# Optimization experiments

Hardware: AMD Instinct MI355X
Metric: run time of the kernel (lower is better)

## Reference

```python
import jax, jax.numpy as jnp
import numpy as np

B, D, L, E, R = 16384, 2048, 3, 8, 64


def setup_inputs() -> dict:
    key = jax.random.key(0)
    k1, k2, k3, k4 = jax.random.split(key, 4)
    scale = 1.0 / np.sqrt(D)  # ~ PyTorch Linear default init scale
    X0 = jax.random.normal(k1, (B, D), dtype=jnp.float32)
    U = jax.random.normal(k2, (L, E, R, D), dtype=jnp.float32) * scale
    V = jax.random.normal(k3, (L, E, R, D), dtype=jnp.float32) * scale
    Wg = jax.random.normal(k4, (L, E, D), dtype=jnp.float32) * scale
    bg = jnp.zeros((L, E), dtype=jnp.float32)
    return {"X0": X0, "U": U, "V": V, "Wg": Wg, "bg": bg}


def reference(X0, U, V, Wg, bg):
    # X0: (B, D); U, V: (L, E, R, D); Wg: (L, E, D); bg: (L, E)
    Xi = X0
    num_layers = U.shape[0]
    for l in range(num_layers):  # small fixed layer count
        gate = jax.nn.softmax(jnp.einsum('bd,ed->be', Xi, Wg[l]) + bg[l], axis=1)  # (B, E)
        Uo = jnp.einsum('bd,erd->ber', Xi, U[l])  # (B, E, R)
        Vo = jnp.einsum('bd,erd->ber', Xi, V[l])  # (B, E, R)
        expert_out = jnp.sum(Uo * Vo, axis=2)     # (B, E) low-rank bilinear forms
        xw = jnp.sum(expert_out * gate, axis=1, keepdims=True)  # (B, 1)
        Xi = Xi + X0 * xw  # residual cross update (dropout=0, eval mode)
    return Xi
```

## Files before the change

### kernel.cpp

```cpp
#include <hip/hip_runtime.h>
#include <hip/hip_bf16.h>

#define BDIM 16384
#define DDIM 2048
#define LNUM 3
#define ENUM 8
#define NP 24

#define BM 256
#define BK 64
#define NT (DDIM / BK)

typedef _Float16 f16x8 __attribute__((ext_vector_type(8)));
typedef _Float16 f16x4 __attribute__((ext_vector_type(4)));
typedef float f32x4 __attribute__((ext_vector_type(4)));

__global__ void cvt_w_kernel(const float* __restrict__ U, const float* __restrict__ V,
                             const float* __restrict__ Wg,
                             _Float16* __restrict__ Wh, _Float16* __restrict__ Wgh) {
    if (blockIdx.x >= 6144) {
        int f = (int)((blockIdx.x - 6144) * blockDim.x + threadIdx.x);
        float4 v = ((const float4*)Wg)[f];
        f16x4 h = { (_Float16)v.x, (_Float16)v.y, (_Float16)v.z, (_Float16)v.w };
        ((f16x4*)Wgh)[f] = h;
        return;
    }
    size_t f = (size_t)blockIdx.x * blockDim.x + threadIdx.x;
    size_t elem = f * 4;
    int d   = (int)(elem & (DDIM - 1));
    int row = (int)((elem >> 11) & 127);
    int p   = (int)(elem >> 18);
    const float* src = (row < 64)
        ? (U + ((size_t)(p * 64 + row) * DDIM + d))
        : (V + ((size_t)(p * 64 + (row - 64)) * DDIM + d));
    float4 v = *(const float4*)src;
    f16x4 h = { (_Float16)v.x, (_Float16)v.y, (_Float16)v.z, (_Float16)v.w };
    ((f16x4*)Wh)[f] = h;
}

__global__ void cvt_x_kernel(const float* __restrict__ X0, _Float16* __restrict__ X0h) {
    size_t f = (size_t)blockIdx.x * blockDim.x + threadIdx.x;
    float4 v = ((const float4*)X0)[f];
    f16x4 h = { (_Float16)v.x, (_Float16)v.y, (_Float16)v.z, (_Float16)v.w };
    ((f16x4*)X0h)[f] = h;
}

__global__ __launch_bounds__(512, 2) void gemm_t_kernel(
    const _Float16* __restrict__ Ah,
    const _Float16* __restrict__ Bh,
    const _Float16* __restrict__ Wgh,
    float* __restrict__ T,
    float* __restrict__ G)
{
    const int by   = blockIdx.y;
    const int m0   = blockIdx.x * BM;
    const int tid  = (int)threadIdx.x;
    const int wave = tid >> 6;
    const int lane = tid & 63;
    const int wm   = wave >> 1;
    const int wn   = wave & 1;
    const int mlane = lane & 15;
    const int quad  = lane >> 4;
    const bool gateblk = (by == 12);

    __shared__ _Float16 Ls[2][2][BM * BK];

    const _Float16* aptr[4];
    const _Float16* bptr[4];
#pragma unroll
    for (int q = 0; q < 4; ++q) {
        int idx = q * 512 + tid;
        int row = idx >> 3;
        int c   = idx & 7;
        int col = ((c ^ (row & 7)) * 8);
        aptr[q] = Ah + (size_t)(m0 + row) * DDIM + col;
        int s = row >> 7;
        int brow = row & 127;
        const _Float16* base;
        int br;
        if (gateblk) {
            base = Wgh;
            br = (s == 0 && brow < NP) ? brow : (brow & 15);
        } else {
            base = Bh + (size_t)(2 * by + s) * 128 * DDIM;
            br = brow;
        }
        bptr[q] = base + (size_t)br * DDIM + col;
    }

    f32x4 acc[4][8];
#pragma unroll
    for (int i = 0; i < 4; ++i)
#pragma unroll
        for (int j = 0; j < 8; ++j) acc[i][j] = (f32x4){0.f, 0.f, 0.f, 0.f};

#pragma unroll
    for (int tt = 0; tt < 2; ++tt) {
#pragma unroll
        for (int q = 0; q < 4; ++q)
            __builtin_amdgcn_global_load_lds(
                (const __attribute__((address_space(1))) void*)(aptr[q] + tt * BK),
                (__attribute__((address_space(3))) void*)&Ls[tt][0][(q * 512 + wave * 64) * 8],
                16, 0, 0);
#pragma unroll
        for (int q = 0; q < 4; ++q)
            __builtin_amdgcn_global_load_lds(
                (const __attribute__((address_space(1))) void*)(bptr[q] + tt * BK),
                (__attribute__((address_space(3))) void*)&Ls[tt][1][(q * 512 + wave * 64) * 8],
                16, 0, 0);
    }

    int cur = 0;
    for (int t = 0; t < NT; ++t) {
        if (t < NT - 1) asm volatile("s_waitcnt vmcnt(8)" ::: "memory");
        else            asm volatile("s_waitcnt vmcnt(0)" ::: "memory");
        __builtin_amdgcn_s_barrier();

        const _Float16* Asc = &Ls[cur][0][0];
        const _Float16* Bsc = &Ls[cur][1][0];

        f16x8 a0[4], a1[4], bx[4], by8[4];
#pragma unroll
        for (int mi = 0; mi < 4; ++mi) {
            int row = wm * 64 + mi * 16 + mlane;
            a0[mi] = *(const f16x8*)&Asc[row * BK + ((quad ^ (row & 7)) * 8)];
        }
#pragma unroll
        for (int ni = 0; ni < 4; ++ni) {
            int row = wn * 128 + ni * 16 + mlane;
            bx[ni] = *(const f16x8*)&Bsc[row * BK + ((quad ^ (row & 7)) * 8)];
        }
#pragma unroll
        for (int ni = 0; ni < 4; ++ni) {
            int row = wn * 128 + (ni + 4) * 16 + mlane;
            by8[ni] = *(const f16x8*)&Bsc[row * BK + ((quad ^ (row & 7)) * 8)];
        }
        __builtin_amdgcn_s_setprio(1);
#pragma unroll
        for (int mi = 0; mi < 4; ++mi)
#pragma unroll
            for (int ni = 0; ni < 4; ++ni)
                acc[mi][ni] = __builtin_amdgcn_mfma_f32_16x16x32_f16(
                    a0[mi], bx[ni], acc[mi][ni], 0, 0, 0);
        __builtin_amdgcn_s_setprio(0);

#pragma unroll
        for (int mi = 0; mi < 4; ++mi) {
            int row = wm * 64 + mi * 16 + mlane;
            a1[mi] = *(const f16x8*)&Asc[row * BK + (((4 + quad) ^ (row & 7)) * 8)];
        }
#pragma unroll
        for (int ni = 0; ni < 4; ++ni) {
            int row = wn * 128 + ni * 16 + mlane;
            bx[ni] = *(const f16x8*)&Bsc[row * BK + (((4 + quad) ^ (row & 7)) * 8)];
        }
        __builtin_amdgcn_s_setprio(1);
#pragma unroll
        for (int mi = 0; mi < 4; ++mi)
#pragma unroll
            for (int ni = 0; ni < 4; ++ni)
                acc[mi][ni + 4] = __builtin_amdgcn_mfma_f32_16x16x32_f16(
                    a0[mi], by8[ni], acc[mi][ni + 4], 0, 0, 0);
        __builtin_amdgcn_s_setprio(0);

#pragma unroll
        for (int ni = 0; ni < 4; ++ni) {
            int row = wn * 128 + (ni + 4) * 16 + mlane;
            by8[ni] = *(const f16x8*)&Bsc[row * BK + (((4 + quad) ^ (row & 7)) * 8)];
        }
        __builtin_amdgcn_s_setprio(1);
#pragma unroll
        for (int mi = 0; mi < 4; ++mi)
#pragma unroll
            for (int ni = 0; ni < 4; ++ni)
                acc[mi][ni] = __builtin_amdgcn_mfma_f32_16x16x32_f16(
                    a1[mi], bx[ni], acc[mi][ni], 0, 0, 0);
        __builtin_amdgcn_s_setprio(0);

        __builtin_amdgcn_s_setprio(1);
#pragma unroll
        for (int mi = 0; mi < 4; ++mi)
#pragma unroll
            for (int ni = 0; ni < 4; ++ni)
                acc[mi][ni + 4] = __builtin_amdgcn_mfma_f32_16x16x32_f16(
                    a1[mi], by8[ni], acc[mi][ni + 4], 0, 0, 0);
        __builtin_amdgcn_s_setprio(0);

        __builtin_amdgcn_s_barrier();
        if (t + 2 < NT) {
            int k0 = (t + 2) * BK;
#pragma unroll
            for (int q = 0; q < 4; ++q)
                __builtin_amdgcn_global_load_lds(
                    (const __attribute__((address_space(1))) void*)(aptr[q] + k0),
                    (__attribute__((address_space(3))) void*)&Ls[cur][0][(q * 512 + wave * 64) * 8],
                    16, 0, 0);
#pragma unroll
            for (int q = 0; q < 4; ++q)
                __builtin_amdgcn_global_load_lds(
                    (const __attribute__((address_space(1))) void*)(bptr[q] + k0),
                    (__attribute__((address_space(3))) void*)&Ls[cur][1][(q * 512 + wave * 64) * 8],
                    16, 0, 0);
        }
        cur ^= 1;
    }

    if (gateblk) {
        if (wn == 1) return;
#pragma unroll
        for (int mi = 0; mi < 4; ++mi)
#pragma unroll
            for (int ni = 0; ni < 2; ++ni) {
                int col = ni * 16 + mlane;
                if (col < NP) {
#pragma unroll
                    for (int j = 0; j < 4; ++j) {
                        int m = wm * 64 + mi * 16 + quad * 4 + j;
                        G[(size_t)col * BDIM + (m0 + m)] = acc[mi][ni][j];
                    }
                }
            }
    } else {
        const int p = 2 * by + wn;
#pragma unroll
        for (int mi = 0; mi < 4; ++mi) {
#pragma unroll
            for (int j = 0; j < 4; ++j) {
                float tp = 0.f;
#pragma unroll
                for (int ni = 0; ni < 4; ++ni)
                    tp += acc[mi][ni][j] * acc[mi][ni + 4][j];
                tp += __shfl_xor(tp, 1);
                tp += __shfl_xor(tp, 2);
                tp += __shfl_xor(tp, 4);
                tp += __shfl_xor(tp, 8);
                if (mlane == 0) {
                    int m = wm * 64 + mi * 16 + quad * 4 + j;
                    T[(size_t)p * BDIM + (m0 + m)] = tp;
                }
            }
        }
    }
}

__global__ void epilogue_kernel(const _Float16* __restrict__ X0h,
                                const float* __restrict__ T,
                                const float* __restrict__ G,
                                const float* __restrict__ bg,
                                float* __restrict__ out) {
    __shared__ float s_sh[16];
    const int b0 = blockIdx.x * 16;
    const int tid = (int)threadIdx.x;
    if (tid < 16) {
        int b = b0 + tid;
        float s = 1.f;
#pragma unroll
        for (int l = 0; l < LNUM; ++l) {
            float logit[ENUM];
            float mx = -1e30f;
#pragma unroll
            for (int e = 0; e < ENUM; ++e) {
                int j = l * ENUM + e;
                float g = s * G[(size_t)j * BDIM + b] + bg[j];
                logit[e] = g;
                mx = fmaxf(mx, g);
            }
            float den = 0.f, num = 0.f;
            float s2 = s * s;
#pragma unroll
            for (int e = 0; e < ENUM; ++e) {
                int j = l * ENUM + e;
                float w = __expf(logit[e] - mx);
                den += w;
                num += w * (s2 * T[(size_t)j * BDIM + b]);
            }
            s += num / den;
        }
        s_sh[tid] = s;
    }
    __syncthreads();
    const int nf4 = DDIM / 4;
    for (int idx = tid; idx < 16 * nf4; idx += 256) {
        int r = idx >> 9;
        int c = idx & (nf4 - 1);
        float s = s_sh[r];
        f16x4 h = ((const f16x4*)(X0h + (size_t)(b0 + r) * DDIM))[c];
        float4 x = { s * (float)h[0], s * (float)h[1], s * (float)h[2], s * (float)h[3] };
        ((float4*)(out + (size_t)(b0 + r) * DDIM))[c] = x;
    }
}

extern "C" void kernel_launch(void* const* d_in, const int* in_sizes, int n_in,
                              void* d_out, int out_size, void* d_ws, size_t ws_size,
                              hipStream_t stream) {
    const float* X0 = (const float*)d_in[0];
    const float* U  = (const float*)d_in[1];
    const float* V  = (const float*)d_in[2];
    const float* Wg = (const float*)d_in[3];
    const float* bg = (const float*)d_in[4];
    float* out = (float*)d_out;

    char* ws = (char*)d_ws;
    _Float16* X0h = (_Float16*)ws;
    _Float16* Wh  = (_Float16*)(ws + 67108864ull);
    _Float16* Wgh = (_Float16*)(ws + 79691776ull);
    float* T      = (float*)(ws + 79790080ull);
    float* G      = (float*)(ws + 81362944ull);

    cvt_w_kernel<<<dim3(6144 + 48), dim3(256), 0, stream>>>(U, V, Wg, Wh, Wgh);
    cvt_x_kernel<<<dim3((BDIM * DDIM / 4) / 256), dim3(256), 0, stream>>>(X0, X0h);
    gemm_t_kernel<<<dim3(BDIM / BM, 13), dim3(512), 0, stream>>>(X0h, Wh, Wgh, T, G);
    epilogue_kernel<<<dim3(BDIM / 16), dim3(256), 0, stream>>>(X0h, T, G, bg, out);
}
```

Before: 490.5 us.

## Move gate projection from GEMM grid into epilogue kernel via MFMA

Drops the 13th block-row of the main GEMM that computed the gate logits, along with the Wg fp16 conversion and the G buffer. Each epilogue block now computes its 16 rows' gate logits with a single wave running MFMA over the X0h rows it already reads, converting Wg to fp16 on the fly into LDS. This removes one of thirteen GEMM block columns and the G round-trip through global memory. In exchange, every epilogue block re-reads and converts all of Wg and serialises a small GEMM on one wave, and the larger LDS footprint may lower occupancy.

```diff
diff --git a/kernel.cpp b/kernel.cpp
--- a/kernel.cpp
+++ b/kernel.cpp
@@ -16,15 +16,7 @@
 typedef float f32x4 __attribute__((ext_vector_type(4)));
 
 __global__ void cvt_w_kernel(const float* __restrict__ U, const float* __restrict__ V,
-                             const float* __restrict__ Wg,
-                             _Float16* __restrict__ Wh, _Float16* __restrict__ Wgh) {
-    if (blockIdx.x >= 6144) {
-        int f = (int)((blockIdx.x - 6144) * blockDim.x + threadIdx.x);
-        float4 v = ((const float4*)Wg)[f];
-        f16x4 h = { (_Float16)v.x, (_Float16)v.y, (_Float16)v.z, (_Float16)v.w };
-        ((f16x4*)Wgh)[f] = h;
-        return;
-    }
+                             _Float16* __restrict__ Wh) {
     size_t f = (size_t)blockIdx.x * blockDim.x + threadIdx.x;
     size_t elem = f * 4;
     int d   = (int)(elem & (DDIM - 1));
@@ -48,9 +40,7 @@
 __global__ __launch_bounds__(512, 2) void gemm_t_kernel(
     const _Float16* __restrict__ Ah,
     const _Float16* __restrict__ Bh,
-    const _Float16* __restrict__ Wgh,
-    float* __restrict__ T,
-    float* __restrict__ G)
+    float* __restrict__ T)
 {
     const int by   = blockIdx.y;
     const int m0   = blockIdx.x * BM;
@@ -61,7 +51,6 @@
     const int wn   = wave & 1;
     const int mlane = lane & 15;
     const int quad  = lane >> 4;
-    const bool gateblk = (by == 12);
 
     __shared__ _Float16 Ls[2][2][BM * BK];
 
@@ -76,16 +65,7 @@
         aptr[q] = Ah + (size_t)(m0 + row) * DDIM + col;
         int s = row >> 7;
         int brow = row & 127;
-        const _Float16* base;
-        int br;
-        if (gateblk) {
-            base = Wgh;
-            br = (s == 0 && brow < NP) ? brow : (brow & 15);
-        } else {
-            base = Bh + (size_t)(2 * by + s) * 128 * DDIM;
-            br = brow;
-        }
-        bptr[q] = base + (size_t)br * DDIM + col;
+        bptr[q] = Bh + (size_t)(2 * by + s) * 128 * DDIM + (size_t)brow * DDIM + col;
     }
 
     f32x4 acc[4][8];
@@ -205,52 +185,92 @@
         cur ^= 1;
     }
 
-    if (gateblk) {
-        if (wn == 1) return;
-#pragma unroll
-        for (int mi = 0; mi < 4; ++mi)
-#pragma unroll
-            for (int ni = 0; ni < 2; ++ni) {
-                int col = ni * 16 + mlane;
-                if (col < NP) {
-#pragma unroll
-                    for (int j = 0; j < 4; ++j) {
-                        int m = wm * 64 + mi * 16 + quad * 4 + j;
-                        G[(size_t)col * BDIM + (m0 + m)] = acc[mi][ni][j];
-                    }
-                }
+    const int p = 2 * by + wn;
+#pragma unroll
+    for (int mi = 0; mi < 4; ++mi) {
+#pragma unroll
+        for (int j = 0; j < 4; ++j) {
+            float tp = 0.f;
+#pragma unroll
+            for (int ni = 0; ni < 4; ++ni)
+                tp += acc[mi][ni][j] * acc[mi][ni + 4][j];
+            tp += __shfl_xor(tp, 1);
+            tp += __shfl_xor(tp, 2);
+            tp += __shfl_xor(tp, 4);
+            tp += __shfl_xor(tp, 8);
+            if (mlane == 0) {
+                int m = wm * 64 + mi * 16 + quad * 4 + j;
+                T[(size_t)p * BDIM + (m0 + m)] = tp;
             }
-    } else {
-        const int p = 2 * by + wn;
-#pragma unroll
-        for (int mi = 0; mi < 4; ++mi) {
-#pragma unroll
-            for (int j = 0; j < 4; ++j) {
-                float tp = 0.f;
-#pragma unroll
-                for (int ni = 0; ni < 4; ++ni)
-                    tp += acc[mi][ni][j] * acc[mi][ni + 4][j];
-                tp += __shfl_xor(tp, 1);
-                tp += __shfl_xor(tp, 2);
-                tp += __shfl_xor(tp, 4);
-                tp += __shfl_xor(tp, 8);
-                if (mlane == 0) {
-                    int m = wm * 64 + mi * 16 + quad * 4 + j;
-                    T[(size_t)p * BDIM + (m0 + m)] = tp;
-                }
-            }
-        }
-    }
-}
-
-__global__ void epilogue_kernel(const _Float16* __restrict__ X0h,
-                                const float* __restrict__ T,
-                                const float* __restrict__ G,
-                                const float* __restrict__ bg,
-                                float* __restrict__ out) {
+        }
+    }
+}
+
+__global__ __launch_bounds__(256) void epilogue_kernel(
+    const _Float16* __restrict__ X0h,
+    const float* __restrict__ T,
+    const float* __restrict__ Wg,
+    const float* __restrict__ bg,
+    float* __restrict__ out) {
+    __shared__ _Float16 Xs[16 * 512];
+    __shared__ _Float16 Ws[32 * 512];
+    __shared__ float Gs[16 * NP];
     __shared__ float s_sh[16];
+
     const int b0 = blockIdx.x * 16;
     const int tid = (int)threadIdx.x;
+    const int wave = tid >> 6;
+    const int lane = tid & 63;
+    const int mlane = lane & 15;
+    const int quad = lane >> 4;
+
+#pragma unroll
+    for (int t = tid; t < 512; t += 256)
+        *(f16x8*)&Ws[24 * 512 + t * 8] = (f16x8){0, 0, 0, 0, 0, 0, 0, 0};
+
+    f32x4 g0 = (f32x4){0.f, 0.f, 0.f, 0.f};
+    f32x4 g1 = (f32x4){0.f, 0.f, 0.f, 0.f};
+
+    for (int kc = 0; kc < 4; ++kc) {
+        __syncthreads();
+#pragma unroll
+        for (int t = tid; t < 1024; t += 256) {
+            int r = t >> 6, c = t & 63;
+            f16x8 v = *(const f16x8*)&X0h[(size_t)(b0 + r) * DDIM + kc * 512 + c * 8];
+            *(f16x8*)&Xs[r * 512 + ((c ^ (r & 7)) * 8)] = v;
+        }
+#pragma unroll
+        for (int t = tid; t < 3072; t += 256) {
+            int r = t >> 7, c4 = t & 127;
+            float4 v = *(const float4*)&Wg[(size_t)r * DDIM + kc * 512 + c4 * 4];
+            f16x4 h = { (_Float16)v.x, (_Float16)v.y, (_Float16)v.z, (_Float16)v.w };
+            int chunk = c4 >> 1, half = c4 & 1;
+            *(f16x4*)&Ws[r * 512 + (((chunk ^ (r & 7)) * 2 + half) * 4)] = h;
+        }
+        __syncthreads();
+        if (wave == 0) {
+#pragma unroll
+            for (int ks = 0; ks < 16; ++ks) {
+                int lc = ks * 4 + quad;
+                f16x8 af  = *(const f16x8*)&Xs[mlane * 512 + ((lc ^ (mlane & 7)) * 8)];
+                f16x8 bf0 = *(const f16x8*)&Ws[mlane * 512 + ((lc ^ (mlane & 7)) * 8)];
+                int r1 = 16 + mlane;
+                f16x8 bf1 = *(const f16x8*)&Ws[r1 * 512 + ((lc ^ (r1 & 7)) * 8)];
+                g0 = __builtin_amdgcn_mfma_f32_16x16x32_f16(af, bf0, g0, 0, 0, 0);
+                g1 = __builtin_amdgcn_mfma_f32_16x16x32_f16(af, bf1, g1, 0, 0, 0);
+            }
+        }
+    }
+    if (wave == 0) {
+#pragma unroll
+        for (int j = 0; j < 4; ++j) {
+            int row = quad * 4 + j;
+            Gs[row * NP + mlane] = g0[j];
+            if (mlane < 8) Gs[row * NP + 16 + mlane] = g1[j];
+        }
+    }
+    __syncthreads();
+
     if (tid < 16) {
         int b = b0 + tid;
         float s = 1.f;
@@ -261,7 +281,7 @@
 #pragma unroll
             for (int e = 0; e < ENUM; ++e) {
                 int j = l * ENUM + e;
-                float g = s * G[(size_t)j * BDIM + b] + bg[j];
+                float g = s * Gs[tid * NP + j] + bg[j];
                 logit[e] = g;
                 mx = fmaxf(mx, g);
             }
@@ -303,12 +323,10 @@
     char* ws = (char*)d_ws;
     _Float16* X0h = (_Float16*)ws;
     _Float16* Wh  = (_Float16*)(ws + 67108864ull);
-    _Float16* Wgh = (_Float16*)(ws + 79691776ull);
-    float* T      = (float*)(ws + 79790080ull);
-    float* G      = (float*)(ws + 81362944ull);
-
-    cvt_w_kernel<<<dim3(6144 + 48), dim3(256), 0, stream>>>(U, V, Wg, Wh, Wgh);
+    float* T      = (float*)(ws + 79691776ull);
+
+    cvt_w_kernel<<<dim3((NP * 128 * DDIM / 4) / 256), dim3(256), 0, stream>>>(U, V, Wh);
     cvt_x_kernel<<<dim3((BDIM * DDIM / 4) / 256), dim3(256), 0, stream>>>(X0, X0h);
-    gemm_t_kernel<<<dim3(BDIM / BM, 13), dim3(512), 0, stream>>>(X0h, Wh, Wgh, T, G);
-    epilogue_kernel<<<dim3(BDIM / 16), dim3(256), 0, stream>>>(X0h, T, G, bg, out);
-}
+    gemm_t_kernel<<<dim3(BDIM / BM, 12), dim3(512), 0, stream>>>(X0h, Wh, T);
+    epilogue_kernel<<<dim3(BDIM / 16), dim3(256), 0, stream>>>(X0h, T, Wg, bg, out);
+}
```

Measured after the change: 494.7 us. No clear change (+0.9%).
